# Optimization experiments

Measured on AMD Instinct MI355X. Metric: run time of the kernel, lower is better.

Reference implementation:

```python
import math
import jax, jax.numpy as jnp
import numpy as np

B, T, D = 2, 1024, 768          # batch, seq, hidden
H = 12                          # attention heads
DH_ATT = D // H
PH, NK, TOPK, DHK = 4, 256, 32, 128  # pkm heads, num product keys, topk, key dim
DQ = PH * DHK * 2               # pkm query projection width
EPS = 1e-5


def _ln(x, g, b):
    m = jnp.mean(x, -1, keepdims=True)
    v = jnp.var(x, -1, keepdims=True)
    return (x - m) * jax.lax.rsqrt(v + EPS) * g + b


def setup_inputs() -> dict:
    key = jax.random.key(0)
    k = jax.random.split(key, 8)
    n = lambda i, s, sc=0.02: jax.random.normal(k[i], s, jnp.float32) * sc
    z = lambda s: jnp.zeros(s, jnp.float32)
    o = lambda s: jnp.ones(s, jnp.float32)
    return {
        "hidden_states": jax.random.normal(k[0], (B, T, D), jnp.float32),
        "wq": n(1, (D, D)), "bq": z((D,)),
        "wk": n(2, (D, D)), "bk": z((D,)),
        "wv": n(3, (D, D)), "bv": z((D,)),
        "wo": n(4, (D, D)), "bo": z((D,)),
        "ln1_g": o((D,)), "ln1_b": z((D,)),
        "ln2_g": o((D,)), "ln2_b": z((D,)),
        "pkm_wq": n(5, (D, DQ)),
        "bn_g": o((DQ,)), "bn_b": z((DQ,)),
        "pkm_keys": n(6, (PH, NK, 2, DHK), 1.0 / math.sqrt(DHK)),
        "pkm_values": n(7, (NK * NK, D), 1.0 / math.sqrt(D)),
    }


def reference(hidden_states, wq, bq, wk, bk, wv, bv, wo, bo,
              ln1_g, ln1_b, ln2_g, ln2_b,
              pkm_wq, bn_g, bn_b, pkm_keys, pkm_values):
    x = hidden_states
    # ---- pre-norm self-attention + residual ----
    h = _ln(x, ln1_g, ln1_b)
    q = (h @ wq + bq).reshape(B, T, H, DH_ATT)
    k = (h @ wk + bk).reshape(B, T, H, DH_ATT)
    v = (h @ wv + bv).reshape(B, T, H, DH_ATT)
    scores = jnp.einsum('bqhd,bkhd->bhqk', q, k) / math.sqrt(DH_ATT)
    probs = jax.nn.softmax(scores, axis=-1)
    attn_out = jnp.einsum('bhqk,bkhd->bqhd', probs, v).reshape(B, T, D) @ wo + bo
    x = x + attn_out
    # ---- pre-norm PKM + residual ----
    h = _ln(x, ln2_g, ln2_b)
    qf = (h @ pkm_wq).reshape(B * T, DQ)
    # BatchNorm1d over tokens (training-mode batch stats)
    mu = jnp.mean(qf, 0)
    var = jnp.var(qf, 0)
    qn = (qf - mu) * jax.lax.rsqrt(var + EPS) * bn_g + bn_b
    # split into the two sub-key query halves: [2, n, PH, DHK]
    qh = jnp.stack(jnp.split(qn, 2, axis=-1)).reshape(2, B * T, PH, DHK)
    # distances against both sub-key codebooks: [n, PH, 2, NK]
    dots = jnp.einsum('pnhd,hkpd->nhpk', qh, pkm_keys)
    s, idx = jax.lax.top_k(dots, TOPK)                       # [n, PH, 2, TOPK]
    all_s = (s[:, :, 0, :, None] + s[:, :, 1, None, :]).reshape(B * T, PH, TOPK * TOPK)
    all_i = (idx[:, :, 0, :, None] * NK + idx[:, :, 1, None, :]).reshape(B * T, PH, TOPK * TOPK)
    fs, fpos = jax.lax.top_k(all_s, TOPK)                    # [n, PH, TOPK]
    vi = jnp.take_along_axis(all_i, fpos, axis=-1)           # cartesian indices
    attn = jax.nn.softmax(fs, axis=-1)
    # EmbeddingBag(mode='sum') with per_sample_weights: gather + weighted sum over PH*TOPK
    pkm_out = jnp.einsum('nhk,nhkd->nd', attn, pkm_values[vi]).reshape(B, T, D)
    return x + pkm_out
```

## Files before the change

### kernel.cpp

```cpp
#include <hip/hip_runtime.h>
#include <hip/hip_bf16.h>

#define B_  2
#define T_  1024
#define D_  768
#define H_  12
#define NT  2048
#define DQ_ 1024
#define PH_ 4
#define NK_ 256
#define TK_ 32
#define DHK_ 128
#define QKVLD 2304
#define CVHALF 25165824L
#define NKEYS (PH_ * NK_ * 2 * DHK_)

typedef __attribute__((ext_vector_type(8))) short bf16x8;
typedef __attribute__((ext_vector_type(4))) float f32x4;
typedef __attribute__((ext_vector_type(2))) float f32x2;

static __device__ __forceinline__ unsigned short f2bf(float f) {
    union { float f; unsigned u; } c; c.f = f;
    unsigned r = (c.u + 0x7fffu + ((c.u >> 16) & 1u)) >> 16;
    return (unsigned short)r;
}

static __device__ __forceinline__ float bf2f(unsigned short s) {
    union { unsigned u; float f; } c; c.u = ((unsigned)s) << 16;
    return c.f;
}

__global__ void transpose_kernel(const float* __restrict__ wq, const float* __restrict__ wk,
                                 const float* __restrict__ wv, const float* __restrict__ wo,
                                 const float* __restrict__ pwq, const float* __restrict__ keys,
                                 unsigned short* __restrict__ wqkvT,
                                 unsigned short* __restrict__ woT,
                                 unsigned short* __restrict__ pwqT,
                                 unsigned short* __restrict__ keyB) {
    __shared__ float t[32][33];
    int z = blockIdx.z;
    if (z == 5) {
        long i = (((long)blockIdx.y * 24 + blockIdx.x) * 256 + threadIdx.y * 32 + threadIdx.x) * 2;
        if (i + 1 < NKEYS) { keyB[i] = f2bf(keys[i]); keyB[i + 1] = f2bf(keys[i + 1]); }
        return;
    }
    const float* W; unsigned short* Wt; int N;
    if (z == 0)      { W = wq;  Wt = wqkvT;              N = 768; }
    else if (z == 1) { W = wk;  Wt = wqkvT + 589824;     N = 768; }
    else if (z == 2) { W = wv;  Wt = wqkvT + 2 * 589824; N = 768; }
    else if (z == 3) { W = wo;  Wt = woT;                N = 768; }
    else             { W = pwq; Wt = pwqT;               N = 1024; }
    int k0 = blockIdx.x * 32, n0 = blockIdx.y * 32;
    if (n0 >= N) return;
    int tx = threadIdx.x, ty = threadIdx.y;
#pragma unroll
    for (int i = 0; i < 4; ++i)
        t[ty + 8 * i][tx] = W[(long)(k0 + ty + 8 * i) * N + n0 + tx];
    __syncthreads();
#pragma unroll
    for (int i = 0; i < 4; ++i)
        Wt[(long)(n0 + ty + 8 * i) * 768 + k0 + tx] = f2bf(t[tx][ty + 8 * i]);
}

__global__ __launch_bounds__(256)
void ln_kernel(const float* __restrict__ x, const float* __restrict__ g,
               const float* __restrict__ b, unsigned short* __restrict__ out) {
    int row = blockIdx.x, tid = threadIdx.x;
    const float* xr = x + (long)row * D_;
    float v0 = xr[tid], v1 = xr[tid + 256], v2 = xr[tid + 512];
    float s = v0 + v1 + v2, ss = v0 * v0 + v1 * v1 + v2 * v2;
#pragma unroll
    for (int o = 1; o < 64; o <<= 1) { s += __shfl_xor(s, o); ss += __shfl_xor(ss, o); }
    __shared__ float ps[4], pss[4];
    int wid = tid >> 6, lane = tid & 63;
    if (lane == 0) { ps[wid] = s; pss[wid] = ss; }
    __syncthreads();
    s = ps[0] + ps[1] + ps[2] + ps[3];
    ss = pss[0] + pss[1] + pss[2] + pss[3];
    float mean = s * (1.f / D_);
    float var = ss * (1.f / D_) - mean * mean;
    float rs = rsqrtf(var + 1e-5f);
    unsigned short* orow = out + (long)row * D_;
    orow[tid]       = f2bf((v0 - mean) * rs * g[tid]       + b[tid]);
    orow[tid + 256] = f2bf((v1 - mean) * rs * g[tid + 256] + b[tid + 256]);
    orow[tid + 512] = f2bf((v2 - mean) * rs * g[tid + 512] + b[tid + 512]);
}

__global__ __launch_bounds__(256)
void gemm_kernel(const unsigned short* __restrict__ A, int lda,
                 const unsigned short* __restrict__ Bt, int ldb,
                 const float* __restrict__ bias,
                 const float* __restrict__ bias2,
                 const float* __restrict__ bias3,
                 const float* __restrict__ res,
                 float* __restrict__ outF,
                 unsigned short* __restrict__ outB,
                 int ldc, int K, int zmode,
                 const float* __restrict__ cvin,
                 unsigned char* __restrict__ cvout,
                 long cvbase, int cvy0) {
    if (cvin && (int)blockIdx.y >= cvy0) {
        long stride = (long)(gridDim.y - cvy0) * gridDim.x * 256 * 8;
        long idx = cvbase +
            ((long)((blockIdx.y - cvy0) * gridDim.x + blockIdx.x) * 256 + threadIdx.x) * 8;
        long end = cvbase + CVHALF;
#pragma unroll 2
        for (; idx < end; idx += stride) {
            f32x4 a = *(const f32x4*)(cvin + idx);
            f32x4 b = *(const f32x4*)(cvin + idx + 4);
            int lo = __builtin_amdgcn_cvt_pk_fp8_f32(a[0], a[1], 0, false);
            lo = __builtin_amdgcn_cvt_pk_fp8_f32(a[2], a[3], lo, true);
            int hi = __builtin_amdgcn_cvt_pk_fp8_f32(b[0], b[1], 0, false);
            hi = __builtin_amdgcn_cvt_pk_fp8_f32(b[2], b[3], hi, true);
            *(uint2*)(cvout + idx) = make_uint2((unsigned)lo, (unsigned)hi);
        }
        return;
    }
    if (zmode == 1) {
        int z = blockIdx.z, ph = z >> 1, half = z & 1;
        A    += half * 512 + ph * 128;
        Bt   += ph * 65536 + half * 128;
        outF += ph * 512 + half * 256;
    }
    const int tid = threadIdx.x;
    const int w = tid >> 6, lane = tid & 63;
    const int ls = lane & 15, g = lane >> 4;
    const int m0 = blockIdx.x * 64, n0 = blockIdx.y * 64;

    __shared__ unsigned short As[64][40];
    __shared__ unsigned short Bs[64][40];

    f32x4 acc[4];
#pragma unroll
    for (int c = 0; c < 4; ++c) acc[c] = (f32x4){0.f, 0.f, 0.f, 0.f};

    const int lrow = tid >> 2, lseg = tid & 3;
    const unsigned short* gA = A + (long)(m0 + lrow) * lda + lseg * 8;
    const unsigned short* gB = Bt + (long)(n0 + lrow) * ldb + lseg * 8;

    for (int kt = 0; kt < K; kt += 32) {
        __syncthreads();
        *(int4*)&As[lrow][lseg * 8] = *(const int4*)(gA + kt);
        *(int4*)&Bs[lrow][lseg * 8] = *(const int4*)(gB + kt);
        __syncthreads();
        bf16x8 bfr = *(const bf16x8*)&Bs[w * 16 + ls][g * 8];
#pragma unroll
        for (int c = 0; c < 4; ++c) {
            bf16x8 afr = *(const bf16x8*)&As[c * 16 + ls][g * 8];
            acc[c] = __builtin_amdgcn_mfma_f32_16x16x32_bf16(afr, bfr, acc[c], 0, 0, 0);
        }
    }
#pragma unroll
    for (int c = 0; c < 4; ++c) {
#pragma unroll
        for (int r = 0; r < 4; ++r) {
            int row = m0 + c * 16 + g * 4 + r;
            int col = n0 + w * 16 + ls;
            float v = acc[c][r];
            if (bias) {
                const float* bp = bias; int cc = col;
                if (zmode == 2) {
                    int sel = col >= 1536 ? 2 : (col >= 768 ? 1 : 0);
                    bp = sel == 0 ? bias : (sel == 1 ? bias2 : bias3);
                    cc = col - sel * 768;
                }
                v += bp[cc];
            }
            long off = (long)row * ldc + col;
            if (res)  v += res[off];
            if (outF) outF[off] = v;
            if (outB) outB[off] = f2bf(v);
        }
    }
}

__global__ __launch_bounds__(256)
void attn_mfma_kernel(const unsigned short* __restrict__ qkv,
                      unsigned short* __restrict__ outg) {
    int bh = blockIdx.x, bb = bh / H_, hh = bh % H_;
    int q0 = blockIdx.y * 64;
    int tid = threadIdx.x, wv = tid >> 6, lane = tid & 63;
    int ls = lane & 15, g = lane >> 4;

    __shared__ unsigned short Klds[128 * 64];
    __shared__ unsigned short Vlds[64 * 128];
    __shared__ unsigned short Plds[4][16 * 128];

    const unsigned short* qrow = qkv + (long)(bb * T_ + q0 + wv * 16 + ls) * QKVLD + hh * 64 + g * 8;
    bf16x8 qf0 = *(const bf16x8*)qrow;
    bf16x8 qf1 = *(const bf16x8*)(qrow + 32);

    f32x4 o_acc[4];
#pragma unroll
    for (int nf = 0; nf < 4; ++nf) o_acc[nf] = (f32x4){0.f, 0.f, 0.f, 0.f};
    float mrun[4] = {-1e30f, -1e30f, -1e30f, -1e30f};
    float lrun[4] = {0.f, 0.f, 0.f, 0.f};

    char* pbase = (char*)&Plds[wv][0];

    for (int kt = 0; kt < T_ / 128; ++kt) {
        int kvb = kt * 128;
        __syncthreads();
#pragma unroll
        for (int i = 0; i < 4; ++i) {
            int c = tid + i * 256;
            int kv = c >> 3, dc = c & 7;
            bf16x8 kd = *(const bf16x8*)(qkv + (long)(bb * T_ + kvb + kv) * QKVLD + 768 + hh * 64 + dc * 8);
            *(bf16x8*)((char*)Klds + ((kv * 128 + dc * 16) ^ ((kv & 7) << 4))) = kd;
        }
        {
            int d0 = (tid & 7) * 8, kvq = tid >> 3;
            const unsigned short* vb = qkv + (long)(bb * T_ + kvb + kvq * 4) * QKVLD + 1536 + hh * 64 + d0;
            bf16x8 r0 = *(const bf16x8*)(vb);
            bf16x8 r1 = *(const bf16x8*)(vb + QKVLD);
            bf16x8 r2 = *(const bf16x8*)(vb + 2 * QKVLD);
            bf16x8 r3 = *(const bf16x8*)(vb + 3 * QKVLD);
#pragma unroll
            for (int j = 0; j < 8; ++j) {
                unsigned lo = (unsigned)(unsigned short)r0[j] | ((unsigned)(unsigned short)r1[j] << 16);
                unsigned hi = (unsigned)(unsigned short)r2[j] | ((unsigned)(unsigned short)r3[j] << 16);
                int d = d0 + j;
                *(uint2*)((char*)Vlds + ((d * 256 + kvq * 8) ^ ((d & 7) << 4))) = make_uint2(lo, hi);
            }
        }
        __syncthreads();

        f32x4 sa[8];
#pragma unroll
        for (int f = 0; f < 8; ++f) sa[f] = (f32x4){0.f, 0.f, 0.f, 0.f};
#pragma unroll
        for (int f = 0; f < 8; ++f) {
            int kv = f * 16 + ls;
            bf16x8 b0 = *(const bf16x8*)((char*)Klds + ((kv * 128 + g * 16) ^ ((kv & 7) << 4)));
            bf16x8 b1 = *(const bf16x8*)((char*)Klds + ((kv * 128 + 64 + g * 16) ^ ((kv & 7) << 4)));
            sa[f] = __builtin_amdgcn_mfma_f32_16x16x32_bf16(qf0, b0, sa[f], 0, 0, 0);
            sa[f] = __builtin_amdgcn_mfma_f32_16x16x32_bf16(qf1, b1, sa[f], 0, 0, 0);
        }

        float pw[8][4];
#pragma unroll
        for (int f = 0; f < 8; ++f)
#pragma unroll
            for (int r = 0; r < 4; ++r) pw[f][r] = sa[f][r] * 0.125f;
        float nm[4], fac[4];
#pragma unroll
        for (int r = 0; r < 4; ++r) {
            float m = pw[0][r];
#pragma unroll
            for (int f = 1; f < 8; ++f) m = fmaxf(m, pw[f][r]);
            m = fmaxf(m, __shfl_xor(m, 1));
            m = fmaxf(m, __shfl_xor(m, 2));
            m = fmaxf(m, __shfl_xor(m, 4));
            m = fmaxf(m, __shfl_xor(m, 8));
            nm[r] = fmaxf(mrun[r], m);
            fac[r] = __expf(mrun[r] - nm[r]);
            mrun[r] = nm[r];
        }
#pragma unroll
        for (int r = 0; r < 4; ++r) {
            float s = 0.f;
#pragma unroll
            for (int f = 0; f < 8; ++f) { float e = __expf(pw[f][r] - nm[r]); pw[f][r] = e; s += e; }
            s += __shfl_xor(s, 1); s += __shfl_xor(s, 2);
            s += __shfl_xor(s, 4); s += __shfl_xor(s, 8);
            lrun[r] = lrun[r] * fac[r] + s;
#pragma unroll
            for (int nf = 0; nf < 4; ++nf) o_acc[nf][r] *= fac[r];
        }

#pragma unroll
        for (int f = 0; f < 8; ++f)
#pragma unroll
            for (int r = 0; r < 4; ++r) {
                int qr = g * 4 + r, col = ls + 16 * f;
                *(unsigned short*)(pbase + ((qr * 256 + col * 2) ^ ((qr & 7) << 4))) = f2bf(pw[f][r]);
            }

#pragma unroll
        for (int ks = 0; ks < 4; ++ks) {
            bf16x8 pa = *(const bf16x8*)(pbase + ((ls * 256 + ks * 64 + g * 16) ^ ((ls & 7) << 4)));
#pragma unroll
            for (int nf = 0; nf < 4; ++nf) {
                int d = nf * 16 + ls;
                bf16x8 bv = *(const bf16x8*)((char*)Vlds + ((d * 256 + ks * 64 + g * 16) ^ ((d & 7) << 4)));
                o_acc[nf] = __builtin_amdgcn_mfma_f32_16x16x32_bf16(pa, bv, o_acc[nf], 0, 0, 0);
            }
        }
    }

    float inv[4];
#pragma unroll
    for (int r = 0; r < 4; ++r) inv[r] = 1.f / lrun[r];
#pragma unroll
    for (int nf = 0; nf < 4; ++nf)
#pragma unroll
        for (int r = 0; r < 4; ++r) {
            long row = bb * T_ + q0 + wv * 16 + g * 4 + r;
            outg[row * D_ + hh * 64 + nf * 16 + ls] = f2bf(o_acc[nf][r] * inv[r]);
        }
}

__global__ __launch_bounds__(256)
void bn_part(const float* __restrict__ qf, float* __restrict__ pS, float* __restrict__ pSS) {
    int c = blockIdx.y * 256 + threadIdx.x;
    int r0 = blockIdx.x * 32;
    float s = 0.f, ss = 0.f;
#pragma unroll 4
    for (int r = 0; r < 32; ++r) {
        float v = qf[(long)(r0 + r) * DQ_ + c];
        s += v; ss += v * v;
    }
    pS[(long)blockIdx.x * DQ_ + c] = s;
    pSS[(long)blockIdx.x * DQ_ + c] = ss;
}

__global__ __launch_bounds__(256)
void bn_fin(const float* __restrict__ pS, const float* __restrict__ pSS,
            float* __restrict__ mu, float* __restrict__ rs) {
    int c = blockIdx.x * 256 + threadIdx.x;
    float s = 0.f, ss = 0.f;
#pragma unroll 8
    for (int i = 0; i < 64; ++i) { s += pS[(long)i * DQ_ + c]; ss += pSS[(long)i * DQ_ + c]; }
    float m = s * (1.f / NT);
    float var = ss * (1.f / NT) - m * m;
    mu[c] = m;
    rs[c] = rsqrtf(var + 1e-5f);
}

__global__ __launch_bounds__(256)
void qn_kernel(const float* __restrict__ qf, const float* __restrict__ mu,
               const float* __restrict__ rs, const float* __restrict__ g,
               const float* __restrict__ b, unsigned short* __restrict__ qn) {
    int i = blockIdx.x * 256 + threadIdx.x;
    int c = i & (DQ_ - 1);
    qn[i] = f2bf((qf[i] - mu[c]) * rs[c] * g[c] + b[c]);
}

__global__ __launch_bounds__(256)
void topk_kernel(const float* __restrict__ dots, float* __restrict__ fs, int* __restrict__ vi) {
    static const unsigned short tab[128] = {
        0,1,2,3,4,5,6,7,8,9,10,11,12,13,14,15,16,17,18,19,20,21,22,23,24,25,26,27,28,29,30,31,
        32,33,34,35,36,37,38,39,40,41,42,43,44,45,46,47,
        64,65,66,67,68,69,70,71,72,73,
        96,97,98,99,100,101,102,103,
        128,129,130,131,132,133,
        160,161,162,163,164,
        192,193,194,195,
        224,225,226,227,
        256,257,258,
        288,289,290,
        320,321, 352,353, 384,385, 416,417, 448,449, 480,481,
        512,544,576,608,640,672,704,736,768,800,832,864,896,928,960,992,
        0xFFFF,0xFFFF,0xFFFF,0xFFFF,0xFFFF,0xFFFF,0xFFFF,0xFFFF,0xFFFF
    };
    __shared__ float sv[2][64];
    __shared__ int   sidx[2][64];
    int tid = threadIdx.x, wv = tid >> 6, lane = tid & 63;
    int slot = wv >> 1, half = wv & 1;
    long task = (long)blockIdx.x * 2 + slot;
    const float* d = dots + (task >> 2) * 2048 + (task & 3) * 512 + half * 256;

    float v0 = d[lane], v1 = d[lane + 64], v2 = d[lane + 128], v3 = d[lane + 192];
#pragma unroll 1
    for (int t = 0; t < 32; ++t) {
        float bm = v0; int ba = 0;
        if (v1 > bm) { bm = v1; ba = 1; }
        if (v2 > bm) { bm = v2; ba = 2; }
        if (v3 > bm) { bm = v3; ba = 3; }
        float wm = bm;
#pragma unroll
        for (int o = 32; o >= 1; o >>= 1) wm = fmaxf(wm, __shfl_xor(wm, o));
        unsigned long long msk = __ballot(bm == wm);
        int owner = (int)__builtin_ctzll(msk);
        if (lane == owner) {
            sv[slot][half * 32 + t] = wm;
            sidx[slot][half * 32 + t] = ba * 64 + lane;
            if (ba == 0) v0 = -1e30f;
            else if (ba == 1) v1 = -1e30f;
            else if (ba == 2) v2 = -1e30f;
            else v3 = -1e30f;
        }
    }
    __syncthreads();
    if (half) return;

    unsigned short t0 = tab[lane], t1 = tab[lane + 64];
    float c0 = -1e30f, c1 = -1e30f;
    int id0 = 0, id1 = 0;
    {
        int i = t0 >> 5, j = t0 & 31;
        c0 = sv[slot][i] + sv[slot][32 + j];
        id0 = sidx[slot][i] * NK_ + sidx[slot][32 + j];
    }
    if (t1 != 0xFFFF) {
        int i = t1 >> 5, j = t1 & 31;
        c1 = sv[slot][i] + sv[slot][32 + j];
        id1 = sidx[slot][i] * NK_ + sidx[slot][32 + j];
    }

    float* fo = fs + task * 32;
    int*   vo = vi + task * 32;
#pragma unroll 1
    for (int t = 0; t < 32; ++t) {
        float bm = c0; int sel = 0;
        if (c1 > bm) { bm = c1; sel = 1; }
        float wm = bm;
#pragma unroll
        for (int o = 32; o >= 1; o >>= 1) wm = fmaxf(wm, __shfl_xor(wm, o));
        unsigned long long msk = __ballot(bm == wm);
        int owner = (int)__builtin_ctzll(msk);
        if (lane == owner) {
            fo[t] = wm;
            vo[t] = sel ? id1 : id0;
            if (sel) c1 = -1e30f; else c0 = -1e30f;
        }
    }
}

__global__ __launch_bounds__(384)
void pkm_out_fp8(const float* __restrict__ fs, const int* __restrict__ vi,
                 const unsigned char* __restrict__ vals8, const float* __restrict__ x1,
                 float* __restrict__ outp) {
    int n = blockIdx.x, tid = threadIdx.x;
    __shared__ float w[128];
    __shared__ int   rows[128];
    __shared__ float red[3 * 768];
    if (tid < 128) {
        float e = fs[(long)n * 128 + tid];
        rows[tid] = vi[(long)n * 128 + tid];
        float m = e;
#pragma unroll
        for (int o = 16; o >= 1; o >>= 1) m = fmaxf(m, __shfl_xor(m, o));
        float ex = __expf(e - m);
        float s = ex;
#pragma unroll
        for (int o = 16; o >= 1; o >>= 1) s += __shfl_xor(s, o);
        w[tid] = ex / s;
    }
    __syncthreads();
    int slot = tid / 96, chunk = tid % 96;
    float a0=0.f,a1=0.f,a2=0.f,a3=0.f,a4=0.f,a5=0.f,a6=0.f,a7=0.f;
#pragma unroll 4
    for (int e = 0; e < 32; ++e) {
        int er = e * 4 + slot;
        float wgt = w[er];
        long ro = (long)rows[er] * D_;
        uint2 v = *(const uint2*)(vals8 + ro + chunk * 8);
        f32x2 f0 = __builtin_amdgcn_cvt_pk_f32_fp8((int)v.x, false);
        f32x2 f1 = __builtin_amdgcn_cvt_pk_f32_fp8((int)v.x, true);
        f32x2 f2 = __builtin_amdgcn_cvt_pk_f32_fp8((int)v.y, false);
        f32x2 f3 = __builtin_amdgcn_cvt_pk_f32_fp8((int)v.y, true);
        a0 += wgt * f0[0]; a1 += wgt * f0[1]; a2 += wgt * f1[0]; a3 += wgt * f1[1];
        a4 += wgt * f2[0]; a5 += wgt * f2[1]; a6 += wgt * f3[0]; a7 += wgt * f3[1];
    }
    if (slot > 0) {
        float* rp = &red[(slot - 1) * 768 + chunk * 8];
        rp[0]=a0; rp[1]=a1; rp[2]=a2; rp[3]=a3; rp[4]=a4; rp[5]=a5; rp[6]=a6; rp[7]=a7;
    }
    __syncthreads();
    if (slot == 0) {
        long o = (long)n * D_ + chunk * 8;
        const float* r0 = &red[chunk * 8];
        const float* r1 = &red[768 + chunk * 8];
        const float* r2 = &red[1536 + chunk * 8];
        f32x4 xa = *(const f32x4*)(x1 + o);
        f32x4 xb = *(const f32x4*)(x1 + o + 4);
        f32x4 o1 = { a0 + r0[0] + r1[0] + r2[0] + xa[0], a1 + r0[1] + r1[1] + r2[1] + xa[1],
                     a2 + r0[2] + r1[2] + r2[2] + xa[2], a3 + r0[3] + r1[3] + r2[3] + xa[3] };
        f32x4 o2 = { a4 + r0[4] + r1[4] + r2[4] + xb[0], a5 + r0[5] + r1[5] + r2[5] + xb[1],
                     a6 + r0[6] + r1[6] + r2[6] + xb[2], a7 + r0[7] + r1[7] + r2[7] + xb[3] };
        *(f32x4*)(outp + o) = o1;
        *(f32x4*)(outp + o + 4) = o2;
    }
}

__global__ __launch_bounds__(384)
void pkm_out_f32(const float* __restrict__ fs, const int* __restrict__ vi,
                 const float* __restrict__ values, const float* __restrict__ x1,
                 float* __restrict__ outp) {
    int n = blockIdx.x, tid = threadIdx.x;
    __shared__ float w[128];
    __shared__ int   rows[128];
    __shared__ float red[768];
    if (tid < 128) {
        float e = fs[(long)n * 128 + tid];
        rows[tid] = vi[(long)n * 128 + tid];
        float m = e;
#pragma unroll
        for (int o = 16; o >= 1; o >>= 1) m = fmaxf(m, __shfl_xor(m, o));
        float ex = __expf(e - m);
        float s = ex;
#pragma unroll
        for (int o = 16; o >= 1; o >>= 1) s += __shfl_xor(s, o);
        w[tid] = ex / s;
    }
    __syncthreads();
    int slot = tid / 192, chunk = tid % 192;
    float a0 = 0.f, a1 = 0.f, a2 = 0.f, a3 = 0.f;
#pragma unroll 4
    for (int e = 0; e < 64; ++e) {
        int er = e * 2 + slot;
        float wgt = w[er];
        long ro = (long)rows[er] * D_;
        f32x4 v = *(const f32x4*)(values + ro + chunk * 4);
        a0 += wgt * v[0]; a1 += wgt * v[1]; a2 += wgt * v[2]; a3 += wgt * v[3];
    }
    if (slot == 1) {
        f32x4 t = {a0, a1, a2, a3};
        *(f32x4*)&red[chunk * 4] = t;
    }
    __syncthreads();
    if (slot == 0) {
        f32x4 o = *(const f32x4*)&red[chunk * 4];
        f32x4 xr = *(const f32x4*)(x1 + (long)n * D_ + chunk * 4);
        o[0] += a0 + xr[0]; o[1] += a1 + xr[1]; o[2] += a2 + xr[2]; o[3] += a3 + xr[3];
        *(f32x4*)(outp + (long)n * D_ + chunk * 4) = o;
    }
}

extern "C" void kernel_launch(void* const* d_in, const int* in_sizes, int n_in,
                              void* d_out, int out_size, void* d_ws, size_t ws_size,
                              hipStream_t stream) {
    const float* x    = (const float*)d_in[0];
    const float* wq   = (const float*)d_in[1];
    const float* bq   = (const float*)d_in[2];
    const float* wk   = (const float*)d_in[3];
    const float* bk   = (const float*)d_in[4];
    const float* wv   = (const float*)d_in[5];
    const float* bv   = (const float*)d_in[6];
    const float* wo   = (const float*)d_in[7];
    const float* bo   = (const float*)d_in[8];
    const float* ln1g = (const float*)d_in[9];
    const float* ln1b = (const float*)d_in[10];
    const float* ln2g = (const float*)d_in[11];
    const float* ln2b = (const float*)d_in[12];
    const float* pwq  = (const float*)d_in[13];
    const float* bng  = (const float*)d_in[14];
    const float* bnb  = (const float*)d_in[15];
    const float* keys = (const float*)d_in[16];
    const float* vals = (const float*)d_in[17];
    float* out = (float*)d_out;

    char* p = (char*)d_ws;
    auto alloc = [&](size_t bytes) -> char* {
        char* r = p; p += (bytes + 255) & ~(size_t)255; return r;
    };
    unsigned short* wqkvT = (unsigned short*)alloc((size_t)3 * D_ * D_ * 2);
    unsigned short* woT   = (unsigned short*)alloc((size_t)D_ * D_ * 2);
    unsigned short* pwqT  = (unsigned short*)alloc((size_t)D_ * DQ_ * 2);
    unsigned short* keyB  = (unsigned short*)alloc((size_t)NKEYS * 2);
    unsigned short* h1    = (unsigned short*)alloc((size_t)NT * D_ * 2);
    unsigned short* qkvB  = (unsigned short*)alloc((size_t)NT * QKVLD * 2);
    unsigned short* aout  = (unsigned short*)alloc((size_t)NT * D_ * 2);
    float* x1             = (float*)alloc((size_t)NT * D_ * 4);
    unsigned short* h2    = (unsigned short*)alloc((size_t)NT * D_ * 2);
    float* qf             = (float*)alloc((size_t)NT * DQ_ * 4);
    float* pS             = (float*)alloc((size_t)64 * DQ_ * 4);
    float* pSS            = (float*)alloc((size_t)64 * DQ_ * 4);
    float* mu             = (float*)alloc((size_t)DQ_ * 4);
    float* rs             = (float*)alloc((size_t)DQ_ * 4);
    unsigned short* qnB   = (unsigned short*)alloc((size_t)NT * DQ_ * 2);
    float* dots           = (float*)alloc((size_t)NT * 2048 * 4);
    float* fsb            = (float*)alloc((size_t)NT * PH_ * 32 * 4);
    int*   vib            = (int*)alloc((size_t)NT * PH_ * 32 * 4);

    size_t used = (size_t)(p - (char*)d_ws);
    size_t vbytes = (size_t)NK_ * NK_ * D_;
    bool useTab = (used + vbytes + 256) <= ws_size;
    unsigned char* vals8 = nullptr;
    if (useTab) vals8 = (unsigned char*)alloc(vbytes);

    transpose_kernel<<<dim3(24, 32, 6), dim3(32, 8), 0, stream>>>(
        wq, wk, wv, wo, pwq, keys, wqkvT, woT, pwqT, keyB);

    ln_kernel<<<NT, 256, 0, stream>>>(x, ln1g, ln1b, h1);
    gemm_kernel<<<dim3(32, useTab ? 52 : 36), 256, 0, stream>>>(
        h1, D_, wqkvT, D_, bq, bk, bv, nullptr, nullptr, qkvB, QKVLD, D_, 2,
        useTab ? vals : nullptr, vals8, 0L, 36);
    attn_mfma_kernel<<<dim3(B_ * H_, T_ / 64), 256, 0, stream>>>(qkvB, aout);
    gemm_kernel<<<dim3(32, 12), 256, 0, stream>>>(
        aout, D_, woT, D_, bo, nullptr, nullptr, x, x1, nullptr, D_, D_, 0,
        nullptr, nullptr, 0L, 0);
    ln_kernel<<<NT, 256, 0, stream>>>(x1, ln2g, ln2b, h2);
    gemm_kernel<<<dim3(32, useTab ? 32 : 16), 256, 0, stream>>>(
        h2, D_, pwqT, D_, nullptr, nullptr, nullptr, nullptr, qf, nullptr, DQ_, D_, 0,
        useTab ? vals : nullptr, vals8, CVHALF, 16);
    bn_part<<<dim3(64, 4), 256, 0, stream>>>(qf, pS, pSS);
    bn_fin<<<4, 256, 0, stream>>>(pS, pSS, mu, rs);
    qn_kernel<<<(NT * DQ_) / 256, 256, 0, stream>>>(qf, mu, rs, bng, bnb, qnB);
    gemm_kernel<<<dim3(32, 4, 8), 256, 0, stream>>>(
        qnB, DQ_, keyB, 256, nullptr, nullptr, nullptr, nullptr, dots, nullptr, 2048, DHK_, 1,
        nullptr, nullptr, 0L, 0);
    topk_kernel<<<(NT * PH_) / 2, 256, 0, stream>>>(dots, fsb, vib);
    if (useTab)
        pkm_out_fp8<<<NT, 384, 0, stream>>>(fsb, vib, vals8, x1, out);
    else
        pkm_out_f32<<<NT, 384, 0, stream>>>(fsb, vib, vals, x1, out);
}
```

Before: 269.9 us.

## Prefetch next K/V tile into registers and use lazy softmax rescaling in attention

The attention kernel now issues the global loads for the next 128-key K/V tile into registers right after the LDS barrier, so they overlap the current tile's MFMA and softmax work. The online softmax rescales the accumulators only when the running max grows by more than 8, which skips most exp/multiply rescale work. It also raises wave priority around the MFMA blocks with s_setprio. The cost is higher register pressure from the prefetch buffers, which could lower occupancy, and the lazy rescale leaves the exponentials slightly less well bounded.

```diff
diff --git a/kernel.cpp b/kernel.cpp
--- a/kernel.cpp
+++ b/kernel.cpp
@@ -197,37 +197,43 @@
     float lrun[4] = {0.f, 0.f, 0.f, 0.f};
 
     char* pbase = (char*)&Plds[wv][0];
-
+    const int d0 = (tid & 7) * 8, kvq = tid >> 3;
+
+    bf16x8 kreg[4], vreg[4];
+    auto loadKV = [&](int kvb) {
+#pragma unroll
+        for (int i = 0; i < 4; ++i) {
+            int c = tid + i * 256;
+            kreg[i] = *(const bf16x8*)(qkv + (long)(bb * T_ + kvb + (c >> 3)) * QKVLD + 768 + hh * 64 + (c & 7) * 8);
+        }
+        const unsigned short* vb = qkv + (long)(bb * T_ + kvb + kvq * 4) * QKVLD + 1536 + hh * 64 + d0;
+#pragma unroll
+        for (int i = 0; i < 4; ++i) vreg[i] = *(const bf16x8*)(vb + i * QKVLD);
+    };
+
+    loadKV(0);
     for (int kt = 0; kt < T_ / 128; ++kt) {
-        int kvb = kt * 128;
         __syncthreads();
 #pragma unroll
         for (int i = 0; i < 4; ++i) {
             int c = tid + i * 256;
             int kv = c >> 3, dc = c & 7;
-            bf16x8 kd = *(const bf16x8*)(qkv + (long)(bb * T_ + kvb + kv) * QKVLD + 768 + hh * 64 + dc * 8);
-            *(bf16x8*)((char*)Klds + ((kv * 128 + dc * 16) ^ ((kv & 7) << 4))) = kd;
-        }
-        {
-            int d0 = (tid & 7) * 8, kvq = tid >> 3;
-            const unsigned short* vb = qkv + (long)(bb * T_ + kvb + kvq * 4) * QKVLD + 1536 + hh * 64 + d0;
-            bf16x8 r0 = *(const bf16x8*)(vb);
-            bf16x8 r1 = *(const bf16x8*)(vb + QKVLD);
-            bf16x8 r2 = *(const bf16x8*)(vb + 2 * QKVLD);
-            bf16x8 r3 = *(const bf16x8*)(vb + 3 * QKVLD);
-#pragma unroll
-            for (int j = 0; j < 8; ++j) {
-                unsigned lo = (unsigned)(unsigned short)r0[j] | ((unsigned)(unsigned short)r1[j] << 16);
-                unsigned hi = (unsigned)(unsigned short)r2[j] | ((unsigned)(unsigned short)r3[j] << 16);
-                int d = d0 + j;
-                *(uint2*)((char*)Vlds + ((d * 256 + kvq * 8) ^ ((d & 7) << 4))) = make_uint2(lo, hi);
-            }
+            *(bf16x8*)((char*)Klds + ((kv * 128 + dc * 16) ^ ((kv & 7) << 4))) = kreg[i];
+        }
+#pragma unroll
+        for (int j = 0; j < 8; ++j) {
+            unsigned lo = (unsigned)(unsigned short)vreg[0][j] | ((unsigned)(unsigned short)vreg[1][j] << 16);
+            unsigned hi = (unsigned)(unsigned short)vreg[2][j] | ((unsigned)(unsigned short)vreg[3][j] << 16);
+            int d = d0 + j;
+            *(uint2*)((char*)Vlds + ((d * 256 + kvq * 8) ^ ((d & 7) << 4))) = make_uint2(lo, hi);
         }
         __syncthreads();
+        if (kt + 1 < T_ / 128) loadKV((kt + 1) * 128);
 
         f32x4 sa[8];
 #pragma unroll
         for (int f = 0; f < 8; ++f) sa[f] = (f32x4){0.f, 0.f, 0.f, 0.f};
+        __builtin_amdgcn_s_setprio(1);
 #pragma unroll
         for (int f = 0; f < 8; ++f) {
             int kv = f * 16 + ls;
@@ -236,13 +242,13 @@
             sa[f] = __builtin_amdgcn_mfma_f32_16x16x32_bf16(qf0, b0, sa[f], 0, 0, 0);
             sa[f] = __builtin_amdgcn_mfma_f32_16x16x32_bf16(qf1, b1, sa[f], 0, 0, 0);
         }
+        __builtin_amdgcn_s_setprio(0);
 
         float pw[8][4];
 #pragma unroll
         for (int f = 0; f < 8; ++f)
 #pragma unroll
             for (int r = 0; r < 4; ++r) pw[f][r] = sa[f][r] * 0.125f;
-        float nm[4], fac[4];
 #pragma unroll
         for (int r = 0; r < 4; ++r) {
             float m = pw[0][r];
@@ -252,20 +258,19 @@
             m = fmaxf(m, __shfl_xor(m, 2));
             m = fmaxf(m, __shfl_xor(m, 4));
             m = fmaxf(m, __shfl_xor(m, 8));
-            nm[r] = fmaxf(mrun[r], m);
-            fac[r] = __expf(mrun[r] - nm[r]);
-            mrun[r] = nm[r];
-        }
-#pragma unroll
-        for (int r = 0; r < 4; ++r) {
+            if (m > mrun[r] + 8.f) {
+                float fac = __expf(mrun[r] - m);
+                lrun[r] *= fac;
+#pragma unroll
+                for (int nf = 0; nf < 4; ++nf) o_acc[nf][r] *= fac;
+                mrun[r] = m;
+            }
             float s = 0.f;
 #pragma unroll
-            for (int f = 0; f < 8; ++f) { float e = __expf(pw[f][r] - nm[r]); pw[f][r] = e; s += e; }
+            for (int f = 0; f < 8; ++f) { float e = __expf(pw[f][r] - mrun[r]); pw[f][r] = e; s += e; }
             s += __shfl_xor(s, 1); s += __shfl_xor(s, 2);
             s += __shfl_xor(s, 4); s += __shfl_xor(s, 8);
-            lrun[r] = lrun[r] * fac[r] + s;
-#pragma unroll
-            for (int nf = 0; nf < 4; ++nf) o_acc[nf][r] *= fac[r];
+            lrun[r] += s;
         }
 
 #pragma unroll
@@ -276,6 +281,7 @@
                 *(unsigned short*)(pbase + ((qr * 256 + col * 2) ^ ((qr & 7) << 4))) = f2bf(pw[f][r]);
             }
 
+        __builtin_amdgcn_s_setprio(1);
 #pragma unroll
         for (int ks = 0; ks < 4; ++ks) {
             bf16x8 pa = *(const bf16x8*)(pbase + ((ls * 256 + ks * 64 + g * 16) ^ ((ls & 7) << 4)));
@@ -286,6 +292,7 @@
                 o_acc[nf] = __builtin_amdgcn_mfma_f32_16x16x32_bf16(pa, bv, o_acc[nf], 0, 0, 0);
             }
         }
+        __builtin_amdgcn_s_setprio(0);
     }
 
     float inv[4];
```

Measured after the change: 269.5 us. Within noise of the previous version (-0.2%).
